# Performance work log

Measured on AMD Instinct MI355X. Metric: run time of the kernel, lower is better.

## Reference

```python
import jax, jax.numpy as jnp
import numpy as np

KSIZE = 51  # radius=50 is even -> incremented to 51 in __init__


def _gaussian_1d(ksize):
    # cv2.getGaussianKernel with sigma<=0: sigma = 0.3*((ksize-1)*0.5 - 1) + 0.8
    sigma = 0.3 * ((ksize - 1) * 0.5 - 1) + 0.8
    x = np.arange(ksize, dtype=np.float64) - (ksize - 1) / 2
    g = np.exp(-(x * x) / (2.0 * sigma * sigma))
    g = g / g.sum()
    return g.astype(np.float32)


def _blur(img, kernel1d):
    """Separable Gaussian blur with reflect padding.
    Mathematically identical to the 2D conv with outer(g, g) in the torch code.
    img: (b, c, h, w), kernel1d: (k,)
    """
    k = kernel1d.shape[0]
    p = k // 2
    b, c, h, w = img.shape
    x = jnp.pad(img, ((0, 0), (0, 0), (p, p), (p, p)), mode='reflect')
    x = x.reshape(b * c, 1, h + 2 * p, w + 2 * p)
    # vertical pass then horizontal pass (conv vs correlation irrelevant: symmetric kernel)
    kv = kernel1d.reshape(1, 1, k, 1)
    kh = kernel1d.reshape(1, 1, 1, k)
    dn = ('NCHW', 'OIHW', 'NCHW')
    x = jax.lax.conv_general_dilated(x, kv, (1, 1), 'VALID', dimension_numbers=dn)
    x = jax.lax.conv_general_dilated(x, kh, (1, 1), 'VALID', dimension_numbers=dn)
    return x.reshape(b, c, h, w)


def setup_inputs() -> dict:
    key = jax.random.key(0)
    img = jax.random.uniform(key, (16, 3, 512, 512), dtype=jnp.float32)
    kernel1d = jnp.asarray(_gaussian_1d(KSIZE))
    return {"img": img, "kernel1d": kernel1d}


def reference(img, kernel1d):
    weight = 0.5
    threshold = 10.0
    blur = _blur(img, kernel1d)
    residual = img - blur
    mask = (jnp.abs(residual) * 255.0 > threshold).astype(img.dtype)
    soft_mask = _blur(mask, kernel1d)
    sharp = jnp.clip(img + weight * residual, 0.0, 1.0)
    return soft_mask * sharp + (1.0 - soft_mask) * img
```

## Files before the change

### kernel.cpp

```cpp
#include <hip/hip_runtime.h>
#include <hip/hip_bf16.h>


typedef __attribute__((ext_vector_type(8))) short bf16x8;
typedef __attribute__((ext_vector_type(4))) float f32x4;

constexpr int IMG = 512, NIMG = 48, K = 51, P = 25;
constexpr int CB = 64;
constexpr int RB = 128;
constexpr int WAVES = 8;
constexpr int TR = RB + 2 * P;
constexpr int SCH = 26;
constexpr int SROW = 256;
constexpr int NK = 96;

__device__ __forceinline__ float bf2f(unsigned short u) {
    return __builtin_bit_cast(float, (unsigned)u << 16);
}
__device__ __forceinline__ unsigned short f2bf(float f) {
    unsigned u = __builtin_bit_cast(unsigned, f);
    u += 0x7FFF + ((u >> 16) & 1);
    return (unsigned short)(u >> 16);
}
__device__ __forceinline__ int sidx(int c, int s) {
    return c * SROW + (s ^ ((c & 7) << 3));
}

template <int SRCB, int LOADM, int STOREM>
__global__ __launch_bounds__(512, 8) void pass_kern(const void* __restrict__ srcv,
                                                    const float* __restrict__ img,
                                                    const unsigned short* __restrict__ res,
                                                    void* __restrict__ dstv,
                                                    const float* __restrict__ k1d) {
    __shared__ unsigned short st[CB * SROW];
    __shared__ unsigned short wb[16 * NK];
    const int tid = threadIdx.x, lane = tid & 63;
    const int wv = __builtin_amdgcn_readfirstlane(tid >> 6);
    const int c0 = blockIdx.x * CB;
    const int r0 = blockIdx.y * RB;
    const size_t base = (size_t)blockIdx.z * (IMG * IMG);

#pragma unroll
    for (int e = 0; e < 3; ++e) {
        const int idx = tid + e * 512;
        const int i = idx / NK, r = idx - i * NK;
        const int t = r - i;
        wb[idx] = (t >= 0 && t < K) ? f2bf(k1d[t]) : (unsigned short)0;
    }

    for (int ch = wv; ch < SCH; ch += WAVES) {
        const int s0 = ch * 8;
        unsigned pk[4];
#pragma unroll
        for (int j2 = 0; j2 < 4; ++j2) {
            unsigned short uu[2];
#pragma unroll
            for (int h = 0; h < 2; ++h) {
                const int s = s0 + j2 * 2 + h;
                unsigned short u = 0;
                if (s < TR) {
                    int y = r0 - P + s;
                    const int ya = y < 0 ? -y : y;
                    y = min(ya, 2 * IMG - 2 - y);
                    const size_t si = base + (size_t)y * IMG + c0 + lane;
                    if (SRCB) {
                        u = ((const unsigned short*)srcv)[si];
                        if (LOADM == 1) u = (fabsf(bf2f(u)) * 255.0f > 10.0f) ? 0x3F80 : 0;
                    } else {
                        u = f2bf(((const float*)srcv)[si]);
                    }
                }
                uu[h] = u;
            }
            pk[j2] = (unsigned)uu[0] | ((unsigned)uu[1] << 16);
        }
        *(uint4*)&st[sidx(lane, s0)] = make_uint4(pk[0], pk[1], pk[2], pk[3]);
    }
    __syncthreads();

    const int m = lane & 15, g = lane >> 4;
    bf16x8 afr[3];
#pragma unroll
    for (int rs = 0; rs < 3; ++rs)
        afr[rs] = *(const bf16x8*)&wb[m * NK + rs * 32 + g * 8];

    const int y0 = wv * 16;
#pragma unroll
    for (int ct = 0; ct < 4; ++ct) {
        const int c = ct * 16 + m;
        f32x4 acc = {0.f, 0.f, 0.f, 0.f};
#pragma unroll
        for (int rs = 0; rs < 3; ++rs) {
            const bf16x8 bfr = *(const bf16x8*)&st[sidx(c, y0 + rs * 32 + g * 8)];
            acc = __builtin_amdgcn_mfma_f32_16x16x32_bf16(afr[rs], bfr, acc, 0, 0, 0);
        }
        const int Cg = c0 + c;
        const int Rg = r0 + y0 + g * 4;
        const size_t di = base + (size_t)Cg * IMG + Rg;
        if (STOREM == 0) {
            const unsigned d0 = (unsigned)f2bf(acc[0]) | ((unsigned)f2bf(acc[1]) << 16);
            const unsigned d1 = (unsigned)f2bf(acc[2]) | ((unsigned)f2bf(acc[3]) << 16);
            *(uint2*)&((unsigned short*)dstv)[di] = make_uint2(d0, d1);
        } else if (STOREM == 1) {
            const f32x4 iv = *(const f32x4*)&img[di];
            const unsigned d0 = (unsigned)f2bf(iv[0] - acc[0]) | ((unsigned)f2bf(iv[1] - acc[1]) << 16);
            const unsigned d1 = (unsigned)f2bf(iv[2] - acc[2]) | ((unsigned)f2bf(iv[3] - acc[3]) << 16);
            *(uint2*)&((unsigned short*)dstv)[di] = make_uint2(d0, d1);
        } else {
            const f32x4 iv = *(const f32x4*)&img[di];
            const uint2 rv2 = *(const uint2*)&res[di];
            f32x4 o;
#pragma unroll
            for (int q = 0; q < 4; ++q) {
                const unsigned rw = (q < 2) ? rv2.x : rv2.y;
                const float rvq = bf2f((unsigned short)(rw >> ((q & 1) * 16)));
                float sharp = fmaf(0.5f, rvq, iv[q]);
                sharp = fminf(fmaxf(sharp, 0.f), 1.f);
                o[q] = fmaf(acc[q], sharp - iv[q], iv[q]);
            }
            *(f32x4*)&((float*)dstv)[di] = o;
        }
    }
}

extern "C" void kernel_launch(void* const* d_in, const int* in_sizes, int n_in,
                              void* d_out, int out_size, void* d_ws, size_t ws_size,
                              hipStream_t stream) {
    (void)in_sizes; (void)n_in; (void)out_size; (void)ws_size;
    const float* img = (const float*)d_in[0];
    const float* k1d = (const float*)d_in[1];
    float* out = (float*)d_out;
    unsigned short* vb = (unsigned short*)d_ws;
    unsigned short* rs = (unsigned short*)d_ws + (size_t)NIMG * IMG * IMG;

    const dim3 grid(IMG / CB, IMG / RB, NIMG);

    pass_kern<0, 0, 0><<<grid, 512, 0, stream>>>(img, nullptr, nullptr, vb, k1d);
    pass_kern<1, 0, 1><<<grid, 512, 0, stream>>>(vb, img, nullptr, rs, k1d);
    pass_kern<1, 1, 0><<<grid, 512, 0, stream>>>(rs, nullptr, nullptr, vb, k1d);
    pass_kern<1, 0, 2><<<grid, 512, 0, stream>>>(vb, img, rs, out, k1d);
}
```

Before: 102.5 us.

## Fuse vertical and horizontal blur passes into one 2D-tiled kernel per blur

Replaces the four separate 1D pass launches with two kernels, each doing both the vertical and horizontal Gaussian pass on a 64x64 tile with halo. The vertical result stays in LDS instead of making a global round trip, and the kernel count is halved. The cost is recomputing halo columns, using more LDS per block (with lower occupancy launch bounds), and doing edge reflection per element on border tiles.

```diff
diff --git a/kernel.cpp b/kernel.cpp
--- a/kernel.cpp
+++ b/kernel.cpp
@@ -5,14 +5,14 @@
 typedef __attribute__((ext_vector_type(8))) short bf16x8;
 typedef __attribute__((ext_vector_type(4))) float f32x4;
 
-constexpr int IMG = 512, NIMG = 48, K = 51, P = 25;
-constexpr int CB = 64;
-constexpr int RB = 128;
+constexpr int IMG = 512, NIMG = 48, K = 51;
+constexpr int TILE = 64;
+constexpr int SCOLS = 128;
+constexpr int SROW = 168;
+constexpr int SDATA = 114;
+constexpr int NCH = 18;
+constexpr int VROW = 152;
 constexpr int WAVES = 8;
-constexpr int TR = RB + 2 * P;
-constexpr int SCH = 26;
-constexpr int SROW = 256;
-constexpr int NK = 96;
 
 __device__ __forceinline__ float bf2f(unsigned short u) {
     return __builtin_bit_cast(float, (unsigned)u << 16);
@@ -22,92 +22,118 @@
     u += 0x7FFF + ((u >> 16) & 1);
     return (unsigned short)(u >> 16);
 }
+__device__ __forceinline__ int refl(int i) {
+    i = i < 0 ? -i : i;
+    return i >= IMG ? 2 * IMG - 2 - i : i;
+}
 __device__ __forceinline__ int sidx(int c, int s) {
-    return c * SROW + (s ^ ((c & 7) << 3));
+    return c * SROW + (s ^ ((c & 3) << 3));
 }
 
 template <int SRCB, int LOADM, int STOREM>
-__global__ __launch_bounds__(512, 8) void pass_kern(const void* __restrict__ srcv,
-                                                    const float* __restrict__ img,
-                                                    const unsigned short* __restrict__ res,
-                                                    void* __restrict__ dstv,
-                                                    const float* __restrict__ k1d) {
-    __shared__ unsigned short st[CB * SROW];
-    __shared__ unsigned short wb[16 * NK];
+__global__ __launch_bounds__(512, 4) void fused_kern(const void* __restrict__ srcv,
+                                                     const float* __restrict__ img,
+                                                     const unsigned short* __restrict__ res,
+                                                     void* __restrict__ dstv,
+                                                     const float* __restrict__ k1d) {
+    __shared__ unsigned short st[SCOLS * SROW];
+    __shared__ unsigned short V[TILE * VROW];
     const int tid = threadIdx.x, lane = tid & 63;
     const int wv = __builtin_amdgcn_readfirstlane(tid >> 6);
-    const int c0 = blockIdx.x * CB;
-    const int r0 = blockIdx.y * RB;
+    const int m = lane & 15, g = lane >> 4;
+    const int x0 = blockIdx.x * TILE, y0 = blockIdx.y * TILE;
     const size_t base = (size_t)blockIdx.z * (IMG * IMG);
 
+    bf16x8 a0[3], a1[3];
 #pragma unroll
-    for (int e = 0; e < 3; ++e) {
-        const int idx = tid + e * 512;
-        const int i = idx / NK, r = idx - i * NK;
-        const int t = r - i;
-        wb[idx] = (t >= 0 && t < K) ? f2bf(k1d[t]) : (unsigned short)0;
+    for (int rs = 0; rs < 3; ++rs) {
+#pragma unroll
+        for (int j = 0; j < 8; ++j) {
+            const int i0 = rs * 32 + 8 * g + j - m;
+            a0[rs][j] = ((unsigned)i0 < (unsigned)K) ? (short)f2bf(k1d[i0]) : (short)0;
+            const int i1 = i0 - 1;
+            a1[rs][j] = ((unsigned)i1 < (unsigned)K) ? (short)f2bf(k1d[i1]) : (short)0;
+        }
     }
 
-    for (int ch = wv; ch < SCH; ch += WAVES) {
+    for (int i = tid; i < TILE * 12; i += 512) {
+        const int r = i / 12, c2 = i - r * 12;
+        *(unsigned*)&V[r * VROW + SCOLS + 2 * c2] = 0u;
+    }
+
+    const bool xedge = (blockIdx.x == 0) || (blockIdx.x == IMG / TILE - 1);
+    for (int ch = wv; ch < NCH; ch += WAVES) {
         const int s0 = ch * 8;
-        unsigned pk[4];
+        unsigned p0[4] = {0, 0, 0, 0}, p1[4] = {0, 0, 0, 0};
 #pragma unroll
-        for (int j2 = 0; j2 < 4; ++j2) {
-            unsigned short uu[2];
-#pragma unroll
-            for (int h = 0; h < 2; ++h) {
-                const int s = s0 + j2 * 2 + h;
-                unsigned short u = 0;
-                if (s < TR) {
-                    int y = r0 - P + s;
-                    const int ya = y < 0 ? -y : y;
-                    y = min(ya, 2 * IMG - 2 - y);
-                    const size_t si = base + (size_t)y * IMG + c0 + lane;
-                    if (SRCB) {
-                        u = ((const unsigned short*)srcv)[si];
-                        if (LOADM == 1) u = (fabsf(bf2f(u)) * 255.0f > 10.0f) ? 0x3F80 : 0;
-                    } else {
-                        u = f2bf(((const float*)srcv)[si]);
-                    }
+        for (int h = 0; h < 8; ++h) {
+            const int sy = min(s0 + h, SDATA - 1);
+            const size_t rowb = base + (size_t)refl(y0 - 25 + sy) * IMG;
+            unsigned short u0, u1;
+            if (SRCB == 0) {
+                float v0, v1;
+                if (!xedge) {
+                    const float2 v = *(const float2*)&((const float*)srcv)[rowb + x0 - 26 + 2 * lane];
+                    v0 = v.x; v1 = v.y;
+                } else {
+                    v0 = ((const float*)srcv)[rowb + refl(x0 - 26 + 2 * lane)];
+                    v1 = ((const float*)srcv)[rowb + refl(x0 - 25 + 2 * lane)];
                 }
-                uu[h] = u;
+                u0 = f2bf(v0); u1 = f2bf(v1);
+            } else {
+                if (!xedge) {
+                    const unsigned v = *(const unsigned*)&((const unsigned short*)srcv)[rowb + x0 - 26 + 2 * lane];
+                    u0 = (unsigned short)v; u1 = (unsigned short)(v >> 16);
+                } else {
+                    u0 = ((const unsigned short*)srcv)[rowb + refl(x0 - 26 + 2 * lane)];
+                    u1 = ((const unsigned short*)srcv)[rowb + refl(x0 - 25 + 2 * lane)];
+                }
+                if (LOADM == 1) {
+                    u0 = (fabsf(bf2f(u0)) * 255.0f > 10.0f) ? 0x3F80 : 0;
+                    u1 = (fabsf(bf2f(u1)) * 255.0f > 10.0f) ? 0x3F80 : 0;
+                }
             }
-            pk[j2] = (unsigned)uu[0] | ((unsigned)uu[1] << 16);
+            p0[h >> 1] |= (unsigned)u0 << ((h & 1) * 16);
+            p1[h >> 1] |= (unsigned)u1 << ((h & 1) * 16);
         }
-        *(uint4*)&st[sidx(lane, s0)] = make_uint4(pk[0], pk[1], pk[2], pk[3]);
+        *(uint4*)&st[sidx(2 * lane, s0)]     = make_uint4(p0[0], p0[1], p0[2], p0[3]);
+        *(uint4*)&st[sidx(2 * lane + 1, s0)] = make_uint4(p1[0], p1[1], p1[2], p1[3]);
     }
     __syncthreads();
 
-    const int m = lane & 15, g = lane >> 4;
-    bf16x8 afr[3];
 #pragma unroll
-    for (int rs = 0; rs < 3; ++rs)
-        afr[rs] = *(const bf16x8*)&wb[m * NK + rs * 32 + g * 8];
-
-    const int y0 = wv * 16;
-#pragma unroll
-    for (int ct = 0; ct < 4; ++ct) {
-        const int c = ct * 16 + m;
+    for (int k4 = 0; k4 < 4; ++k4) {
+        const int t = wv + 8 * k4;
+        const int xs = t & 7, ys = t >> 3;
         f32x4 acc = {0.f, 0.f, 0.f, 0.f};
 #pragma unroll
         for (int rs = 0; rs < 3; ++rs) {
-            const bf16x8 bfr = *(const bf16x8*)&st[sidx(c, y0 + rs * 32 + g * 8)];
-            acc = __builtin_amdgcn_mfma_f32_16x16x32_bf16(afr[rs], bfr, acc, 0, 0, 0);
+            const bf16x8 b = *(const bf16x8*)&st[sidx(16 * xs + m, 16 * ys + rs * 32 + 8 * g)];
+            acc = __builtin_amdgcn_mfma_f32_16x16x32_bf16(a0[rs], b, acc, 0, 0, 0);
         }
-        const int Cg = c0 + c;
-        const int Rg = r0 + y0 + g * 4;
-        const size_t di = base + (size_t)Cg * IMG + Rg;
-        if (STOREM == 0) {
-            const unsigned d0 = (unsigned)f2bf(acc[0]) | ((unsigned)f2bf(acc[1]) << 16);
-            const unsigned d1 = (unsigned)f2bf(acc[2]) | ((unsigned)f2bf(acc[3]) << 16);
-            *(uint2*)&((unsigned short*)dstv)[di] = make_uint2(d0, d1);
-        } else if (STOREM == 1) {
-            const f32x4 iv = *(const f32x4*)&img[di];
+#pragma unroll
+        for (int q = 0; q < 4; ++q)
+            V[(16 * ys + 4 * g + q) * VROW + 16 * xs + m] = f2bf(acc[q]);
+    }
+    __syncthreads();
+
+#pragma unroll
+    for (int k2 = 0; k2 < 2; ++k2) {
+        const int t = wv + 8 * k2;
+        const int xs = t & 3, ys = t >> 2;
+        f32x4 acc = {0.f, 0.f, 0.f, 0.f};
+#pragma unroll
+        for (int rs = 0; rs < 3; ++rs) {
+            const bf16x8 b = *(const bf16x8*)&V[(16 * ys + m) * VROW + 16 * xs + rs * 32 + 8 * g];
+            acc = __builtin_amdgcn_mfma_f32_16x16x32_bf16(a1[rs], b, acc, 0, 0, 0);
+        }
+        const size_t di = base + (size_t)(y0 + 16 * ys + m) * IMG + (x0 + 16 * xs + 4 * g);
+        const f32x4 iv = *(const f32x4*)&img[di];
+        if (STOREM == 1) {
             const unsigned d0 = (unsigned)f2bf(iv[0] - acc[0]) | ((unsigned)f2bf(iv[1] - acc[1]) << 16);
             const unsigned d1 = (unsigned)f2bf(iv[2] - acc[2]) | ((unsigned)f2bf(iv[3] - acc[3]) << 16);
             *(uint2*)&((unsigned short*)dstv)[di] = make_uint2(d0, d1);
         } else {
-            const f32x4 iv = *(const f32x4*)&img[di];
             const uint2 rv2 = *(const uint2*)&res[di];
             f32x4 o;
 #pragma unroll
@@ -130,13 +156,10 @@
     const float* img = (const float*)d_in[0];
     const float* k1d = (const float*)d_in[1];
     float* out = (float*)d_out;
-    unsigned short* vb = (unsigned short*)d_ws;
-    unsigned short* rs = (unsigned short*)d_ws + (size_t)NIMG * IMG * IMG;
+    unsigned short* rs = (unsigned short*)d_ws;
 
-    const dim3 grid(IMG / CB, IMG / RB, NIMG);
+    const dim3 grid(IMG / TILE, IMG / TILE, NIMG);
 
-    pass_kern<0, 0, 0><<<grid, 512, 0, stream>>>(img, nullptr, nullptr, vb, k1d);
-    pass_kern<1, 0, 1><<<grid, 512, 0, stream>>>(vb, img, nullptr, rs, k1d);
-    pass_kern<1, 1, 0><<<grid, 512, 0, stream>>>(rs, nullptr, nullptr, vb, k1d);
-    pass_kern<1, 0, 2><<<grid, 512, 0, stream>>>(vb, img, rs, out, k1d);
+    fused_kern<0, 0, 1><<<grid, 512, 0, stream>>>(img, img, nullptr, rs, k1d);
+    fused_kern<1, 1, 2><<<grid, 512, 0, stream>>>(rs, img, rs, out, k1d);
 }
```

New measurement: 159.0 us. 1.55x slower.
